# Kernel tuning notes

Hardware: AMD Instinct MI355X
Metric: run time of the kernel (lower is better)

Reference implementation:

```python
import jax, jax.numpy as jnp
import numpy as np

N = 50000
E = 800000
IN_CH = 2048
HID = 64      # hidden per head
HEADS = 4
OUT = 128
NEG_SLOPE = 0.2  # PyG GATv2Conv default
BN_EPS = 1e-5


def setup_inputs() -> dict:
    key = jax.random.key(0)
    ks = jax.random.split(key, 16)
    s = 0.02
    return {
        "x": jax.random.normal(ks[0], (N, IN_CH), jnp.float32),
        "edge_index": jax.random.randint(ks[1], (2, E), 0, N, jnp.int64),
        # conv1: in 2048 -> 4 heads x 64 (concat)
        "W1l": jax.random.normal(ks[2], (IN_CH, HEADS * HID), jnp.float32) * s,
        "W1r": jax.random.normal(ks[3], (IN_CH, HEADS * HID), jnp.float32) * s,
        "att1": jax.random.normal(ks[4], (HEADS, HID), jnp.float32) * s,
        "b1": jnp.zeros((HEADS * HID,), jnp.float32),
        # conv2: in 256 -> 1 head x 128 (no concat)
        "W2l": jax.random.normal(ks[5], (HEADS * HID, OUT), jnp.float32) * s,
        "W2r": jax.random.normal(ks[6], (HEADS * HID, OUT), jnp.float32) * s,
        "att2": jax.random.normal(ks[7], (1, OUT), jnp.float32) * s,
        "b2": jnp.zeros((OUT,), jnp.float32),
        # projection head: Linear -> BatchNorm1d -> ReLU -> Linear
        "pw1": jax.random.normal(ks[8], (OUT, OUT), jnp.float32) * s,
        "pb1": jnp.zeros((OUT,), jnp.float32),
        "gamma": jnp.ones((OUT,), jnp.float32),
        "beta": jnp.zeros((OUT,), jnp.float32),
        "pw2": jax.random.normal(ks[9], (OUT, OUT), jnp.float32) * s,
        "pb2": jnp.zeros((OUT,), jnp.float32),
    }


def gatv2_layer(x, src, dst, Wl, Wr, att, bias, heads, out_ch, concat):
    n = x.shape[0]
    xl = (x @ Wl).reshape(n, heads, out_ch)  # source-side transform
    xr = (x @ Wr).reshape(n, heads, out_ch)  # target-side transform
    # GATv2 score: a^T LeakyReLU(Wl x_j + Wr x_i) per edge, per head
    m = xl[src] + xr[dst]                              # [Et, H, C]
    e = jnp.einsum('ehc,hc->eh', jax.nn.leaky_relu(m, NEG_SLOPE), att)  # [Et, H]
    # segment softmax over incoming edges of each dst node
    emax = jax.ops.segment_max(e, dst, num_segments=n)  # [N, H]
    a = jnp.exp(e - emax[dst])
    denom = jax.ops.segment_sum(a, dst, num_segments=n)
    alpha = a / denom[dst]                              # [Et, H]
    out = jax.ops.segment_sum(alpha[:, :, None] * xl[src], dst, num_segments=n)  # [N, H, C]
    out = out.reshape(n, heads * out_ch) if concat else out.mean(axis=1)
    return out + bias


def reference(x, edge_index, W1l, W1r, att1, b1, W2l, W2r, att2, b2,
              pw1, pb1, gamma, beta, pw2, pb2):
    n = x.shape[0]
    loop = jnp.arange(n, dtype=edge_index.dtype)
    src = jnp.concatenate([edge_index[0], loop])  # add self loops (PyG default)
    dst = jnp.concatenate([edge_index[1], loop])

    h = gatv2_layer(x, src, dst, W1l, W1r, att1, b1, HEADS, HID, concat=True)
    h = jax.nn.relu(h)
    h = gatv2_layer(h, src, dst, W2l, W2r, att2, b2, 1, OUT, concat=False)

    # projection head (BatchNorm1d with batch statistics, training-mode math)
    h = h @ pw1 + pb1
    mu = h.mean(axis=0)
    var = h.var(axis=0)
    h = (h - mu) * jax.lax.rsqrt(var + BN_EPS) * gamma + beta
    h = jax.nn.relu(h)
    return h @ pw2 + pb2
```

## Files before the change

### kernel.cpp

```cpp
#include <hip/hip_runtime.h>
#include <hip/hip_bf16.h>
#include <cstdint>
#include <cstddef>

#define NN 50000
#define NE 800000
#define ETOT (NN + NE)

typedef float f32x4 __attribute__((ext_vector_type(4)));
typedef short s16x8 __attribute__((ext_vector_type(8)));

__device__ __forceinline__ unsigned short f2bf(float f) {
  unsigned u = __float_as_uint(f);
  u += 0x7FFFu + ((u >> 16) & 1u);
  return (unsigned short)(u >> 16);
}
__device__ __forceinline__ float bf2f(unsigned short u) {
  return __uint_as_float(((unsigned)u) << 16);
}
__device__ __forceinline__ unsigned cvtpk(float lo, float hi) {
  unsigned r;
  asm("v_cvt_pk_bf16_f32 %0, %1, %2" : "=v"(r) : "v"(lo), "v"(hi));
  return r;
}
typedef const __attribute__((address_space(1))) void* gas_t;
typedef __attribute__((address_space(3))) void* las_t;
__device__ __forceinline__ void gload_lds16(const void* g, void* l) {
  __builtin_amdgcn_global_load_lds((gas_t)g, (las_t)l, 16, 0, 0);
}

__global__ void detect_i64(const void* __restrict__ ei, int* __restrict__ flag) {
  const long long v = ((const long long*)ei)[threadIdx.x];
  const bool ok = (v >= 0 && v < NN);
  const unsigned long long m = __ballot(ok);
  if (threadIdx.x == 0) *flag = (m == ~0ULL) ? 1 : 0;
}
__device__ __forceinline__ void load_edge(const void* __restrict__ ei, int is64,
                                          int eidx, int& src, int& dst) {
  if (eidx >= NE) { src = dst = eidx - NE; return; }
  if (is64) {
    src = (int)((const long long*)ei)[eidx];
    dst = (int)((const long long*)ei)[NE + eidx];
  } else {
    src = ((const int*)ei)[eidx];
    dst = ((const int*)ei)[NE + eidx];
  }
}

__global__ __launch_bounds__(256) void csr_hist(
    const void* __restrict__ ei, const int* __restrict__ flag, int* __restrict__ cnt)
{
  const int e = blockIdx.x * 256 + threadIdx.x;
  if (e >= ETOT) return;
  int src, dst;
  load_edge(ei, *flag, e, src, dst);
  atomicAdd(&cnt[dst], 1);
}

__global__ __launch_bounds__(256) void scan_blk(
    const int* __restrict__ cnt, int* __restrict__ rp1, int* __restrict__ bsum)
{
  const int tid = threadIdx.x, lane = tid & 63, w = tid >> 6;
  const int i = blockIdx.x * 256 + tid;
  int s = (i < NN) ? cnt[i] : 0;
  #pragma unroll
  for (int off = 1; off < 64; off <<= 1) {
    int t = __shfl_up(s, off);
    if (lane >= off) s += t;
  }
  __shared__ int wsum[4];
  if (lane == 63) wsum[w] = s;
  __syncthreads();
  int add = 0;
  #pragma unroll
  for (int k = 0; k < 4; ++k) if (k < w) add += wsum[k];
  s += add;
  if (i < NN) rp1[i] = s;
  if (tid == 255) bsum[blockIdx.x] = s;
}

__global__ __launch_bounds__(256) void scan_tops(int* __restrict__ bsum, int nb)
{
  const int tid = threadIdx.x, lane = tid & 63, w = tid >> 6;
  int s = (tid < nb) ? bsum[tid] : 0;
  #pragma unroll
  for (int off = 1; off < 64; off <<= 1) {
    int t = __shfl_up(s, off);
    if (lane >= off) s += t;
  }
  __shared__ int wsum[4];
  if (lane == 63) wsum[w] = s;
  __syncthreads();
  int add = 0;
  #pragma unroll
  for (int k = 0; k < 4; ++k) if (k < w) add += wsum[k];
  s += add;
  if (tid < nb) bsum[tid] = s;
}

__global__ __launch_bounds__(256) void scan_add(
    const int* __restrict__ bsum, int* __restrict__ rowptr)
{
  const int i = blockIdx.x * 256 + threadIdx.x;
  if (i == 0) rowptr[0] = 0;
  if (i < NN) rowptr[i + 1] += (blockIdx.x > 0) ? bsum[blockIdx.x - 1] : 0;
}

__global__ __launch_bounds__(256) void csr_scatter(
    const void* __restrict__ ei, const int* __restrict__ flag,
    int* __restrict__ cur, int* __restrict__ colv)
{
  const int e = blockIdx.x * 256 + threadIdx.x;
  if (e >= ETOT) return;
  int src, dst;
  load_edge(ei, *flag, e, src, dst);
  const int pos = atomicAdd(&cur[dst], 1);
  colv[pos] = src;
}

template<bool AF32>
__global__ __launch_bounds__(512) void gemm8(
    const void* __restrict__ Av, const unsigned short* __restrict__ BT,
    void* __restrict__ Cv, const float* __restrict__ bias,
    int M, int K, int Ncols, int out_bf16, int nbx, int nwg)
{
  constexpr int ABYTES = AF32 ? 256 * 32 * 4 : 256 * 32 * 2;
  __shared__ __align__(16) unsigned char Araw[2][ABYTES];
  __shared__ __align__(16) unsigned short Bs[2][128 * 32];

  int bid = blockIdx.x;
  {
    const int q = nwg >> 3, r = nwg & 7;
    const int xcd = bid & 7, idx = bid >> 3;
    bid = (xcd < r ? xcd * (q + 1) : r * (q + 1) + (xcd - r) * q) + idx;
  }
  const int bx = bid % nbx, by = bid / nbx;
  const int row0 = by * 256, col0 = bx * 128;
  const int tid = threadIdx.x, wave = tid >> 6, lane = tid & 63;
  const int l16 = lane & 15, lq = lane >> 4;
  const int wr = wave >> 1, wc = wave & 1;

  const unsigned short* Abf = (const unsigned short*)Av;
  const float*          Af  = (const float*)Av;

  f32x4 acc[4][4];
  #pragma unroll
  for (int i = 0; i < 4; ++i)
    #pragma unroll
    for (int j = 0; j < 4; ++j)
      #pragma unroll
      for (int r = 0; r < 4; ++r) acc[i][j][r] = 0.f;

  auto stageA = [&](int buf, int k0) {
    if constexpr (AF32) {
      #pragma unroll
      for (int j = 0; j < 4; ++j) {
        const int c = tid + 512 * j;
        const int row = c >> 3;
        const int kg = (c & 7) ^ (row & 7);
        int gr = row0 + row; if (gr >= M) gr = M - 1;
        gload_lds16(Af + (size_t)gr * K + k0 + kg * 4, Araw[buf] + c * 16);
      }
    } else {
      #pragma unroll
      for (int j = 0; j < 2; ++j) {
        const int c = tid + 512 * j;
        const int row = c >> 2, part = c & 3;
        int gr = row0 + row; if (gr >= M) gr = M - 1;
        gload_lds16(Abf + (size_t)gr * K + k0 + part * 8, Araw[buf] + c * 16);
      }
    }
  };
  auto stageB = [&](int buf, int k0) {
    const int c = tid;
    const int row = c >> 2, part = c & 3;
    gload_lds16(BT + (size_t)(col0 + row) * K + k0 + part * 8,
                (unsigned char*)Bs[buf] + c * 16);
  };

  const int nt = K >> 5;
  stageA(0, 0);
  stageB(0, 0);
  __syncthreads();

  for (int t = 0; t < nt; ++t) {
    const int cur = t & 1, nxt = cur ^ 1;
    if (t + 1 < nt) {
      stageA(nxt, (t + 1) << 5);
      stageB(nxt, (t + 1) << 5);
    }

    s16x8 af[4], bf[4];
    if constexpr (AF32) {
      const float* Ab = (const float*)Araw[cur];
      #pragma unroll
      for (int f = 0; f < 4; ++f) {
        const int row = wr * 64 + f * 16 + l16;
        const int s0 = (row << 3) + ((2 * lq)     ^ (row & 7));
        const int s1 = (row << 3) + ((2 * lq + 1) ^ (row & 7));
        const float4 f0 = *(const float4*)(Ab + s0 * 4);
        const float4 f1 = *(const float4*)(Ab + s1 * 4);
        uint4 w;
        w.x = cvtpk(f0.x, f0.y); w.y = cvtpk(f0.z, f0.w);
        w.z = cvtpk(f1.x, f1.y); w.w = cvtpk(f1.z, f1.w);
        af[f] = *(s16x8*)&w;
      }
    } else {
      const unsigned short* Ab = (const unsigned short*)Araw[cur];
      #pragma unroll
      for (int f = 0; f < 4; ++f)
        af[f] = *(const s16x8*)&Ab[(wr * 64 + f * 16 + l16) * 32 + lq * 8];
    }
    #pragma unroll
    for (int f = 0; f < 4; ++f)
      bf[f] = *(const s16x8*)&Bs[cur][(wc * 64 + f * 16 + l16) * 32 + lq * 8];

    #pragma unroll
    for (int fm = 0; fm < 4; ++fm)
      #pragma unroll
      for (int fn = 0; fn < 4; ++fn)
        acc[fm][fn] = __builtin_amdgcn_mfma_f32_16x16x32_bf16(af[fm], bf[fn], acc[fm][fn], 0, 0, 0);

    __syncthreads();
  }

  float bv[4];
  #pragma unroll
  for (int fn = 0; fn < 4; ++fn)
    bv[fn] = bias ? bias[col0 + wc * 64 + fn * 16 + l16] : 0.f;

  #pragma unroll
  for (int fm = 0; fm < 4; ++fm) {
    #pragma unroll
    for (int r = 0; r < 4; ++r) {
      const int row = row0 + wr * 64 + fm * 16 + lq * 4 + r;
      if (row < M) {
        #pragma unroll
        for (int fn = 0; fn < 4; ++fn) {
          const int col = col0 + wc * 64 + fn * 16 + l16;
          const float v = acc[fm][fn][r] + bv[fn];
          if (out_bf16) ((unsigned short*)Cv)[(size_t)row * Ncols + col] = f2bf(v);
          else          ((float*)Cv)[(size_t)row * Ncols + col] = v;
        }
      }
    }
  }
}

template<int AMODE, bool BNS>
__global__ __launch_bounds__(256) void gemm_t(
    const void* __restrict__ Av, const unsigned short* __restrict__ BT,
    void* __restrict__ Cv, const float* __restrict__ bias,
    const float* __restrict__ abn, float* __restrict__ bnsum,
    int M, int K, int Ncols, int out_bf16, int nbx, int nwg)
{
  constexpr bool AF32 = (AMODE > 0);
  __shared__ __align__(16) unsigned char Araw[2][AF32 ? 128 * 32 * 4 : 128 * 32 * 2];
  __shared__ __align__(16) unsigned short Bs[2][128 * 32];

  int bid = blockIdx.x;
  {
    const int q = nwg >> 3, r = nwg & 7;
    const int xcd = bid & 7, idx = bid >> 3;
    bid = (xcd < r ? xcd * (q + 1) : r * (q + 1) + (xcd - r) * q) + idx;
  }
  const int bx = bid % nbx, by = bid / nbx;
  const int row0 = by * 128, col0 = bx * 128;
  const int tid = threadIdx.x, wave = tid >> 6, lane = tid & 63;
  const int l16 = lane & 15, lq = lane >> 4;
  const int wr = wave >> 1, wc = wave & 1;

  const unsigned short* Abf = (const unsigned short*)Av;
  const float*          Af  = (const float*)Av;

  f32x4 acc[4][4];
  #pragma unroll
  for (int i = 0; i < 4; ++i)
    #pragma unroll
    for (int j = 0; j < 4; ++j)
      #pragma unroll
      for (int r = 0; r < 4; ++r) acc[i][j][r] = 0.f;

  auto stageA = [&](int buf, int k0) {
    if constexpr (AF32) {
      #pragma unroll
      for (int j = 0; j < 4; ++j) {
        const int c = tid + 256 * j;
        const int row = c >> 3;
        const int kg = (c & 7) ^ (row & 7);
        int gr = row0 + row; if (gr >= M) gr = M - 1;
        gload_lds16(Af + (size_t)gr * K + k0 + kg * 4, Araw[buf] + c * 16);
      }
    } else {
      #pragma unroll
      for (int j = 0; j < 2; ++j) {
        const int c = tid + 256 * j;
        const int row = c >> 2, part = c & 3;
        int gr = row0 + row; if (gr >= M) gr = M - 1;
        gload_lds16(Abf + (size_t)gr * K + k0 + part * 8, Araw[buf] + c * 16);
      }
    }
  };
  auto stageB = [&](int buf, int k0) {
    #pragma unroll
    for (int j = 0; j < 2; ++j) {
      const int c = tid + 256 * j;
      const int row = c >> 2, part = c & 3;
      gload_lds16(BT + (size_t)(col0 + row) * K + k0 + part * 8,
                  (unsigned char*)Bs[buf] + c * 16);
    }
  };

  const int nt = K >> 5;
  stageA(0, 0);
  stageB(0, 0);
  __syncthreads();

  for (int t = 0; t < nt; ++t) {
    const int cur = t & 1, nxt = cur ^ 1;
    if (t + 1 < nt) {
      stageA(nxt, (t + 1) << 5);
      stageB(nxt, (t + 1) << 5);
    }

    s16x8 af[4], bf[4];
    if constexpr (AF32) {
      const float* Ab = (const float*)Araw[cur];
      float sc[8], sh[8];
      if constexpr (AMODE == 2) {
        const int kb = (t << 5) + lq * 8;
        *(float4*)&sc[0] = *(const float4*)(abn + kb);
        *(float4*)&sc[4] = *(const float4*)(abn + kb + 4);
        *(float4*)&sh[0] = *(const float4*)(abn + K + kb);
        *(float4*)&sh[4] = *(const float4*)(abn + K + kb + 4);
      }
      #pragma unroll
      for (int f = 0; f < 4; ++f) {
        const int row = wr * 64 + f * 16 + l16;
        const int s0 = (row << 3) + ((2 * lq)     ^ (row & 7));
        const int s1 = (row << 3) + ((2 * lq + 1) ^ (row & 7));
        float4 f0 = *(const float4*)(Ab + s0 * 4);
        float4 f1 = *(const float4*)(Ab + s1 * 4);
        if constexpr (AMODE == 2) {
          f0.x = fmaxf(f0.x * sc[0] + sh[0], 0.f);
          f0.y = fmaxf(f0.y * sc[1] + sh[1], 0.f);
          f0.z = fmaxf(f0.z * sc[2] + sh[2], 0.f);
          f0.w = fmaxf(f0.w * sc[3] + sh[3], 0.f);
          f1.x = fmaxf(f1.x * sc[4] + sh[4], 0.f);
          f1.y = fmaxf(f1.y * sc[5] + sh[5], 0.f);
          f1.z = fmaxf(f1.z * sc[6] + sh[6], 0.f);
          f1.w = fmaxf(f1.w * sc[7] + sh[7], 0.f);
        }
        uint4 w;
        w.x = cvtpk(f0.x, f0.y); w.y = cvtpk(f0.z, f0.w);
        w.z = cvtpk(f1.x, f1.y); w.w = cvtpk(f1.z, f1.w);
        af[f] = *(s16x8*)&w;
      }
    } else {
      const unsigned short* Ab = (const unsigned short*)Araw[cur];
      #pragma unroll
      for (int f = 0; f < 4; ++f)
        af[f] = *(const s16x8*)&Ab[(wr * 64 + f * 16 + l16) * 32 + lq * 8];
    }
    #pragma unroll
    for (int f = 0; f < 4; ++f)
      bf[f] = *(const s16x8*)&Bs[cur][(wc * 64 + f * 16 + l16) * 32 + lq * 8];

    #pragma unroll
    for (int fm = 0; fm < 4; ++fm)
      #pragma unroll
      for (int fn = 0; fn < 4; ++fn)
        acc[fm][fn] = __builtin_amdgcn_mfma_f32_16x16x32_bf16(af[fm], bf[fn], acc[fm][fn], 0, 0, 0);

    __syncthreads();
  }

  float bv[4];
  #pragma unroll
  for (int fn = 0; fn < 4; ++fn)
    bv[fn] = bias ? bias[col0 + wc * 64 + fn * 16 + l16] : 0.f;

  float sl[4] = {0.f, 0.f, 0.f, 0.f}, ql[4] = {0.f, 0.f, 0.f, 0.f};

  #pragma unroll
  for (int fm = 0; fm < 4; ++fm) {
    #pragma unroll
    for (int r = 0; r < 4; ++r) {
      const int row = row0 + wr * 64 + fm * 16 + lq * 4 + r;
      if (row < M) {
        #pragma unroll
        for (int fn = 0; fn < 4; ++fn) {
          const int col = col0 + wc * 64 + fn * 16 + l16;
          const float v = acc[fm][fn][r] + bv[fn];
          if (BNS) { sl[fn] += v; ql[fn] += v * v; }
          if (out_bf16) ((unsigned short*)Cv)[(size_t)row * Ncols + col] = f2bf(v);
          else          ((float*)Cv)[(size_t)row * Ncols + col] = v;
        }
      }
    }
  }
  if constexpr (BNS) {
    __shared__ float csum[128], cqsum[128];
    if (tid < 128) { csum[tid] = 0.f; cqsum[tid] = 0.f; }
    __syncthreads();
    #pragma unroll
    for (int fn = 0; fn < 4; ++fn) {
      float s = sl[fn], q = ql[fn];
      s += __shfl_down(s, 16); s += __shfl_down(s, 32);
      q += __shfl_down(q, 16); q += __shfl_down(q, 32);
      if (lq == 0) {
        atomicAdd(&csum[wc * 64 + fn * 16 + l16], s);
        atomicAdd(&cqsum[wc * 64 + fn * 16 + l16], q);
      }
    }
    __syncthreads();
    if (tid < 128) {
      atomicAdd(&bnsum[col0 + tid], csum[tid]);
      atomicAdd(&bnsum[128 + col0 + tid], cqsum[tid]);
    }
  }
}

__global__ __launch_bounds__(256) void node_conv1(
    const unsigned short* __restrict__ H1, const int* __restrict__ rowptr,
    const int* __restrict__ colv, const float* __restrict__ att,
    const float* __restrict__ b1, unsigned short* __restrict__ out)
{
  const int tid = threadIdx.x, wave = tid >> 6, lane = tid & 63;
  const int half = lane >> 5, l32 = lane & 31;
  const int node = blockIdx.x * 8 + wave * 2 + half;
  if (node >= NN) return;
  const int ch8 = l32 * 8;
  float xr[8], at[8];
  {
    const s16x8 t = *(const s16x8*)&H1[(size_t)node * 512 + 256 + ch8];
    #pragma unroll
    for (int j = 0; j < 8; ++j) {
      xr[j] = bf2f(((const unsigned short*)&t)[j]);
      at[j] = att[ch8 + j];
    }
  }
  float m = -1e30f, s = 0.f;
  float a[8] = {0.f, 0.f, 0.f, 0.f, 0.f, 0.f, 0.f, 0.f};
  const int beg = rowptr[node], end = rowptr[node + 1];
  s16x8 xa = *(const s16x8*)&H1[(size_t)colv[beg] * 512 + ch8];
  s16x8 xb = (beg + 1 < end) ? *(const s16x8*)&H1[(size_t)colv[beg + 1] * 512 + ch8] : xa;
  for (int i = beg; i < end; ++i) {
    const int ip2 = (i + 2 < end) ? i + 2 : end - 1;
    const s16x8 xc = *(const s16x8*)&H1[(size_t)colv[ip2] * 512 + ch8];
    float xv[8];
    #pragma unroll
    for (int j = 0; j < 8; ++j) xv[j] = bf2f(((const unsigned short*)&xa)[j]);
    float e = 0.f;
    #pragma unroll
    for (int j = 0; j < 8; ++j) {
      float mm = xv[j] + xr[j];
      mm = mm > 0.f ? mm : 0.2f * mm;
      e += mm * at[j];
    }
    e += __shfl_xor(e, 1); e += __shfl_xor(e, 2); e += __shfl_xor(e, 4);
    const float mn = fmaxf(m, e);
    const float scx = __expf(m - mn);
    const float w  = __expf(e - mn);
    s = s * scx + w;
    #pragma unroll
    for (int j = 0; j < 8; ++j) a[j] = a[j] * scx + w * xv[j];
    m = mn;
    xa = xb; xb = xc;
  }
  const float inv = 1.f / s;
  unsigned short ov[8];
  #pragma unroll
  for (int j = 0; j < 8; ++j) ov[j] = f2bf(fmaxf(a[j] * inv + b1[ch8 + j], 0.f));
  *(s16x8*)&out[(size_t)node * 256 + ch8] = *(const s16x8*)ov;
}

__global__ __launch_bounds__(256) void node_conv2(
    const unsigned short* __restrict__ H2, const int* __restrict__ rowptr,
    const int* __restrict__ colv, const float* __restrict__ att,
    const float* __restrict__ b2, unsigned short* __restrict__ out)
{
  const int tid = threadIdx.x, wave = tid >> 6, lane = tid & 63;
  const int qr = lane >> 4, l16 = lane & 15;
  const int node = blockIdx.x * 16 + wave * 4 + qr;
  if (node >= NN) return;
  const int ch8 = l16 * 8;
  float xr[8], at[8];
  {
    const s16x8 t = *(const s16x8*)&H2[(size_t)node * 256 + 128 + ch8];
    #pragma unroll
    for (int j = 0; j < 8; ++j) {
      xr[j] = bf2f(((const unsigned short*)&t)[j]);
      at[j] = att[ch8 + j];
    }
  }
  float m = -1e30f, s = 0.f;
  float a[8] = {0.f, 0.f, 0.f, 0.f, 0.f, 0.f, 0.f, 0.f};
  const int beg = rowptr[node], end = rowptr[node + 1];
  s16x8 xa = *(const s16x8*)&H2[(size_t)colv[beg] * 256 + ch8];
  s16x8 xb = (beg + 1 < end) ? *(const s16x8*)&H2[(size_t)colv[beg + 1] * 256 + ch8] : xa;
  for (int i = beg; i < end; ++i) {
    const int ip2 = (i + 2 < end) ? i + 2 : end - 1;
    const s16x8 xc = *(const s16x8*)&H2[(size_t)colv[ip2] * 256 + ch8];
    float xv[8];
    #pragma unroll
    for (int j = 0; j < 8; ++j) xv[j] = bf2f(((const unsigned short*)&xa)[j]);
    float e = 0.f;
    #pragma unroll
    for (int j = 0; j < 8; ++j) {
      float mm = xv[j] + xr[j];
      mm = mm > 0.f ? mm : 0.2f * mm;
      e += mm * at[j];
    }
    e += __shfl_xor(e, 1); e += __shfl_xor(e, 2);
    e += __shfl_xor(e, 4); e += __shfl_xor(e, 8);
    const float mn = fmaxf(m, e);
    const float scx = __expf(m - mn);
    const float w  = __expf(e - mn);
    s = s * scx + w;
    #pragma unroll
    for (int j = 0; j < 8; ++j) a[j] = a[j] * scx + w * xv[j];
    m = mn;
    xa = xb; xb = xc;
  }
  const float inv = 1.f / s;
  unsigned short ov[8];
  #pragma unroll
  for (int j = 0; j < 8; ++j) ov[j] = f2bf(a[j] * inv + b2[ch8 + j]);
  *(s16x8*)&out[(size_t)node * 128 + ch8] = *(const s16x8*)ov;
}

__global__ __launch_bounds__(256) void wt_cvt_all(
    const float* __restrict__ W1l, const float* __restrict__ W1r, unsigned short* __restrict__ WT1,
    const float* __restrict__ W2l, const float* __restrict__ W2r, unsigned short* __restrict__ WT2,
    const float* __restrict__ pw1, unsigned short* __restrict__ PT1,
    const float* __restrict__ pw2, unsigned short* __restrict__ PT2)
{
  int b = blockIdx.x;
  const float *Wa, *Wb;
  unsigned short* dst;
  int K, halfN, k0, n0;
  if (b < 256)      { Wa = W1l; Wb = W1r; dst = WT1; K = 2048; halfN = 256; k0 = (b & 31) * 64; n0 = (b >> 5) * 64; }
  else if (b < 272) { b -= 256; Wa = W2l; Wb = W2r; dst = WT2; K = 256; halfN = 128; k0 = (b & 3) * 64; n0 = (b >> 2) * 64; }
  else if (b < 276) { b -= 272; Wa = pw1; Wb = pw1; dst = PT1; K = 128; halfN = 128; k0 = (b & 1) * 64; n0 = (b >> 1) * 64; }
  else              { b -= 276; Wa = pw2; Wb = pw2; dst = PT2; K = 128; halfN = 128; k0 = (b & 1) * 64; n0 = (b >> 1) * 64; }
  __shared__ float tile[64][65];
  const int tx = threadIdx.x & 63, ty = threadIdx.x >> 6;
  const float* W = (n0 < halfN) ? Wa : Wb;
  const int nb = (n0 < halfN) ? n0 : n0 - halfN;
  #pragma unroll
  for (int j = 0; j < 16; ++j) {
    const int kl = ty * 16 + j;
    tile[kl][tx] = W[(size_t)(k0 + kl) * halfN + nb + tx];
  }
  __syncthreads();
  #pragma unroll
  for (int j = 0; j < 16; ++j) {
    const int nl = ty * 16 + j;
    dst[(size_t)(n0 + nl) * K + k0 + tx] = f2bf(tile[tx][nl]);
  }
}

__global__ void bn_final(const float* __restrict__ sums, const float* __restrict__ gamma,
                         const float* __restrict__ beta, float* __restrict__ bnp, int M)
{
  const int c = threadIdx.x;
  if (c < 128) {
    const float mu  = sums[c] / (float)M;
    const float var = sums[128 + c] / (float)M - mu * mu;
    const float sc  = gamma[c] * rsqrtf(var + 1e-5f);
    bnp[c] = sc;
    bnp[128 + c] = beta[c] - mu * sc;
  }
}

extern "C" void kernel_launch(void* const* d_in, const int* in_sizes, int n_in,
                              void* d_out, int out_size, void* d_ws, size_t ws_size,
                              hipStream_t stream)
{
  (void)in_sizes; (void)n_in; (void)out_size; (void)ws_size;
  const float* x     = (const float*)d_in[0];
  const void*  ei    = (const void*)d_in[1];
  const float* W1l   = (const float*)d_in[2];
  const float* W1r   = (const float*)d_in[3];
  const float* att1  = (const float*)d_in[4];
  const float* b1    = (const float*)d_in[5];
  const float* W2l   = (const float*)d_in[6];
  const float* W2r   = (const float*)d_in[7];
  const float* att2  = (const float*)d_in[8];
  const float* b2    = (const float*)d_in[9];
  const float* pw1   = (const float*)d_in[10];
  const float* pb1   = (const float*)d_in[11];
  const float* gamma = (const float*)d_in[12];
  const float* beta  = (const float*)d_in[13];
  const float* pw2   = (const float*)d_in[14];
  const float* pb2   = (const float*)d_in[15];

  char* ws = (char*)d_ws;
  unsigned short* H1b   = (unsigned short*)(ws + 0);
  unsigned short* h1b   = (unsigned short*)(ws + 51200000);
  unsigned short* H2b   = (unsigned short*)(ws + 76800000);
  unsigned short* h2b   = (unsigned short*)(ws + 102400000);
  float*          tbuf  = (float*)(ws + 115200000);
  int*            rowptr = (int*)(ws + 153600000);
  int*            cnt    = (int*)(ws + 153800192);
  int*            colv   = (int*)(ws + 154000384);
  unsigned short* WT1    = (unsigned short*)(ws + 157400384);
  unsigned short* WT2    = (unsigned short*)(ws + 159497536);
  unsigned short* PT1    = (unsigned short*)(ws + 159628608);
  unsigned short* PT2    = (unsigned short*)(ws + 159661376);
  float*          bnsum  = (float*)(ws + 159694144);
  float*          bnp    = (float*)(ws + 159695168);
  int*            eflag  = (int*)(ws + 159696192);
  int*            bsum   = (int*)(ws + 159696256);

  hipMemsetAsync(cnt, 0, 200000, stream);
  hipMemsetAsync(bnsum, 0, 1024, stream);

  detect_i64<<<1, 64, 0, stream>>>(ei, eflag);
  wt_cvt_all<<<280, 256, 0, stream>>>(W1l, W1r, WT1, W2l, W2r, WT2, pw1, PT1, pw2, PT2);

  const int ebl = (ETOT + 255) / 256;
  const int nsb = (NN + 255) / 256;
  csr_hist<<<ebl, 256, 0, stream>>>(ei, eflag, cnt);
  scan_blk<<<nsb, 256, 0, stream>>>(cnt, rowptr + 1, bsum);
  scan_tops<<<1, 256, 0, stream>>>(bsum, nsb);
  scan_add<<<nsb, 256, 0, stream>>>(bsum, rowptr);
  hipMemcpyAsync(cnt, rowptr, 200000, hipMemcpyDeviceToDevice, stream);
  csr_scatter<<<ebl, 256, 0, stream>>>(ei, eflag, cnt, colv);

  const int nb256 = (NN + 255) / 256;
  const int nby   = (NN + 127) / 128;

  gemm8<true><<<nb256 * 4, 512, 0, stream>>>(x, WT1, H1b, nullptr, NN, 2048, 512, 1, 4, nb256 * 4);
  node_conv1<<<(NN + 7) / 8, 256, 0, stream>>>(H1b, rowptr, colv, att1, b1, h1b);

  gemm8<false><<<nb256 * 2, 512, 0, stream>>>(h1b, WT2, H2b, nullptr, NN, 256, 256, 1, 2, nb256 * 2);
  node_conv2<<<(NN + 15) / 16, 256, 0, stream>>>(H2b, rowptr, colv, att2, b2, h2b);

  gemm_t<0, true><<<nby, 256, 0, stream>>>(h2b, PT1, tbuf, pb1, nullptr, bnsum, NN, 128, 128, 0, 1, nby);
  bn_final<<<1, 128, 0, stream>>>(bnsum, gamma, beta, bnp, NN);
  gemm_t<2, false><<<nby, 256, 0, stream>>>(tbuf, PT2, (float*)d_out, pb2, bnp, nullptr, NN, 128, 128, 0, 1, nby);
}
```

Before: 526.1 us.

## Sort nodes by in-degree to balance per-wave work in aggregation kernels

Builds a degree histogram during the CSR scan, prefix-sums it into per-degree buckets, and writes a node permutation ordered by in-degree (capped at 255). Both node aggregation kernels then process nodes in this order, so the half-waves or quarter-waves packed into one wave handle nodes with similar edge counts. This is meant to cut divergence, since lanes otherwise idle while waiting for the highest-degree node in their wave. In exchange it adds atomics to a small histogram, an extra indirection per node, and scattered output writes and self-feature reads.

```diff
diff --git a/kernel.cpp b/kernel.cpp
--- a/kernel.cpp
+++ b/kernel.cpp
@@ -29,11 +29,14 @@
   __builtin_amdgcn_global_load_lds((gas_t)g, (las_t)l, 16, 0, 0);
 }
 
-__global__ void detect_i64(const void* __restrict__ ei, int* __restrict__ flag) {
+__global__ void detect_i64(const void* __restrict__ ei, int* __restrict__ flag,
+                           int* __restrict__ dhist) {
   const long long v = ((const long long*)ei)[threadIdx.x];
   const bool ok = (v >= 0 && v < NN);
   const unsigned long long m = __ballot(ok);
   if (threadIdx.x == 0) *flag = (m == ~0ULL) ? 1 : 0;
+  #pragma unroll
+  for (int j = 0; j < 4; ++j) dhist[threadIdx.x * 4 + j] = 0;
 }
 __device__ __forceinline__ void load_edge(const void* __restrict__ ei, int is64,
                                           int eidx, int& src, int& dst) {
@@ -58,11 +61,14 @@
 }
 
 __global__ __launch_bounds__(256) void scan_blk(
-    const int* __restrict__ cnt, int* __restrict__ rp1, int* __restrict__ bsum)
+    const int* __restrict__ cnt, int* __restrict__ rp1, int* __restrict__ bsum,
+    int* __restrict__ dhist)
 {
   const int tid = threadIdx.x, lane = tid & 63, w = tid >> 6;
   const int i = blockIdx.x * 256 + tid;
-  int s = (i < NN) ? cnt[i] : 0;
+  int v = (i < NN) ? cnt[i] : 0;
+  if (i < NN) atomicAdd(&dhist[v < 255 ? v : 255], 1);
+  int s = v;
   #pragma unroll
   for (int off = 1; off < 64; off <<= 1) {
     int t = __shfl_up(s, off);
@@ -79,31 +85,57 @@
   if (tid == 255) bsum[blockIdx.x] = s;
 }
 
-__global__ __launch_bounds__(256) void scan_tops(int* __restrict__ bsum, int nb)
+__global__ __launch_bounds__(256) void scan_tops(
+    int* __restrict__ bsum, int nb, const int* __restrict__ dhist, int* __restrict__ dcur)
 {
   const int tid = threadIdx.x, lane = tid & 63, w = tid >> 6;
-  int s = (tid < nb) ? bsum[tid] : 0;
-  #pragma unroll
-  for (int off = 1; off < 64; off <<= 1) {
-    int t = __shfl_up(s, off);
-    if (lane >= off) s += t;
-  }
   __shared__ int wsum[4];
-  if (lane == 63) wsum[w] = s;
+  {
+    int s = (tid < nb) ? bsum[tid] : 0;
+    #pragma unroll
+    for (int off = 1; off < 64; off <<= 1) {
+      int t = __shfl_up(s, off);
+      if (lane >= off) s += t;
+    }
+    if (lane == 63) wsum[w] = s;
+    __syncthreads();
+    int add = 0;
+    #pragma unroll
+    for (int k = 0; k < 4; ++k) if (k < w) add += wsum[k];
+    s += add;
+    if (tid < nb) bsum[tid] = s;
+  }
   __syncthreads();
-  int add = 0;
-  #pragma unroll
-  for (int k = 0; k < 4; ++k) if (k < w) add += wsum[k];
-  s += add;
-  if (tid < nb) bsum[tid] = s;
+  {
+    const int v = dhist[tid];
+    int s = v;
+    #pragma unroll
+    for (int off = 1; off < 64; off <<= 1) {
+      int t = __shfl_up(s, off);
+      if (lane >= off) s += t;
+    }
+    if (lane == 63) wsum[w] = s;
+    __syncthreads();
+    int add = 0;
+    #pragma unroll
+    for (int k = 0; k < 4; ++k) if (k < w) add += wsum[k];
+    s += add;
+    dcur[tid] = s - v;
+  }
 }
 
 __global__ __launch_bounds__(256) void scan_add(
-    const int* __restrict__ bsum, int* __restrict__ rowptr)
+    const int* __restrict__ bsum, int* __restrict__ rowptr,
+    const int* __restrict__ cnt, int* __restrict__ dcur, int* __restrict__ order)
 {
   const int i = blockIdx.x * 256 + threadIdx.x;
   if (i == 0) rowptr[0] = 0;
-  if (i < NN) rowptr[i + 1] += (blockIdx.x > 0) ? bsum[blockIdx.x - 1] : 0;
+  if (i < NN) {
+    rowptr[i + 1] += (blockIdx.x > 0) ? bsum[blockIdx.x - 1] : 0;
+    const int d = cnt[i] < 255 ? cnt[i] : 255;
+    const int pos = atomicAdd(&dcur[d], 1);
+    order[pos] = i;
+  }
 }
 
 __global__ __launch_bounds__(256) void csr_scatter(
@@ -423,13 +455,15 @@
 
 __global__ __launch_bounds__(256) void node_conv1(
     const unsigned short* __restrict__ H1, const int* __restrict__ rowptr,
-    const int* __restrict__ colv, const float* __restrict__ att,
-    const float* __restrict__ b1, unsigned short* __restrict__ out)
+    const int* __restrict__ colv, const int* __restrict__ order,
+    const float* __restrict__ att, const float* __restrict__ b1,
+    unsigned short* __restrict__ out)
 {
   const int tid = threadIdx.x, wave = tid >> 6, lane = tid & 63;
   const int half = lane >> 5, l32 = lane & 31;
-  const int node = blockIdx.x * 8 + wave * 2 + half;
-  if (node >= NN) return;
+  const int gidx = blockIdx.x * 8 + wave * 2 + half;
+  if (gidx >= NN) return;
+  const int node = order[gidx];
   const int ch8 = l32 * 8;
   float xr[8], at[8];
   {
@@ -477,13 +511,15 @@
 
 __global__ __launch_bounds__(256) void node_conv2(
     const unsigned short* __restrict__ H2, const int* __restrict__ rowptr,
-    const int* __restrict__ colv, const float* __restrict__ att,
-    const float* __restrict__ b2, unsigned short* __restrict__ out)
+    const int* __restrict__ colv, const int* __restrict__ order,
+    const float* __restrict__ att, const float* __restrict__ b2,
+    unsigned short* __restrict__ out)
 {
   const int tid = threadIdx.x, wave = tid >> 6, lane = tid & 63;
   const int qr = lane >> 4, l16 = lane & 15;
-  const int node = blockIdx.x * 16 + wave * 4 + qr;
-  if (node >= NN) return;
+  const int gidx = blockIdx.x * 16 + wave * 4 + qr;
+  if (gidx >= NN) return;
+  const int node = order[gidx];
   const int ch8 = l16 * 8;
   float xr[8], at[8];
   {
@@ -613,19 +649,22 @@
   float*          bnp    = (float*)(ws + 159695168);
   int*            eflag  = (int*)(ws + 159696192);
   int*            bsum   = (int*)(ws + 159696256);
+  int*            dhist  = (int*)(ws + 159697088);
+  int*            dcur   = (int*)(ws + 159698112);
+  int*            order  = (int*)(ws + 159699136);
 
   hipMemsetAsync(cnt, 0, 200000, stream);
   hipMemsetAsync(bnsum, 0, 1024, stream);
 
-  detect_i64<<<1, 64, 0, stream>>>(ei, eflag);
+  detect_i64<<<1, 64, 0, stream>>>(ei, eflag, dhist);
   wt_cvt_all<<<280, 256, 0, stream>>>(W1l, W1r, WT1, W2l, W2r, WT2, pw1, PT1, pw2, PT2);
 
   const int ebl = (ETOT + 255) / 256;
   const int nsb = (NN + 255) / 256;
   csr_hist<<<ebl, 256, 0, stream>>>(ei, eflag, cnt);
-  scan_blk<<<nsb, 256, 0, stream>>>(cnt, rowptr + 1, bsum);
-  scan_tops<<<1, 256, 0, stream>>>(bsum, nsb);
-  scan_add<<<nsb, 256, 0, stream>>>(bsum, rowptr);
+  scan_blk<<<nsb, 256, 0, stream>>>(cnt, rowptr + 1, bsum, dhist);
+  scan_tops<<<1, 256, 0, stream>>>(bsum, nsb, dhist, dcur);
+  scan_add<<<nsb, 256, 0, stream>>>(bsum, rowptr, cnt, dcur, order);
   hipMemcpyAsync(cnt, rowptr, 200000, hipMemcpyDeviceToDevice, stream);
   csr_scatter<<<ebl, 256, 0, stream>>>(ei, eflag, cnt, colv);
 
@@ -633,10 +672,10 @@
   const int nby   = (NN + 127) / 128;
 
   gemm8<true><<<nb256 * 4, 512, 0, stream>>>(x, WT1, H1b, nullptr, NN, 2048, 512, 1, 4, nb256 * 4);
-  node_conv1<<<(NN + 7) / 8, 256, 0, stream>>>(H1b, rowptr, colv, att1, b1, h1b);
+  node_conv1<<<(NN + 7) / 8, 256, 0, stream>>>(H1b, rowptr, colv, order, att1, b1, h1b);
 
   gemm8<false><<<nb256 * 2, 512, 0, stream>>>(h1b, WT2, H2b, nullptr, NN, 256, 256, 1, 2, nb256 * 2);
-  node_conv2<<<(NN + 15) / 16, 256, 0, stream>>>(H2b, rowptr, colv, att2, b2, h2b);
+  node_conv2<<<(NN + 15) / 16, 256, 0, stream>>>(H2b, rowptr, colv, order, att2, b2, h2b);
 
   gemm_t<0, true><<<nby, 256, 0, stream>>>(h2b, PT1, tbuf, pb1, nullptr, bnsum, NN, 128, 128, 0, 1, nby);
   bn_final<<<1, 128, 0, stream>>>(bnsum, gamma, beta, bnp, NN);
```

New measurement: 753.6 us. +43.2%, slower.
